# Optimization experiments

Measured on AMD Instinct MI355X. Metric: run time of the kernel, lower is better.

The kernel has to match this reference:

```python
import jax, jax.numpy as jnp
import numpy as np
from math import factorial

# ---- config (matches init_kwargs) ----
N = 50000                 # batch of nodes/edges
LS = [0, 1, 2]            # l of each irrep block (in1, in2, out all share this)
MUL1, MUL2, MULO = 128, 1, 128
DIM = sum(2 * l + 1 for l in LS)  # 9 basis functions
INSTR = [(0,0,0),(0,1,1),(0,2,2),(1,0,1),(1,1,0),(1,1,1),(1,1,2),(1,2,1),(1,2,2),
         (2,0,2),(2,1,1),(2,1,2),(2,2,0),(2,2,1),(2,2,2)]
PATH_NUMEL = MUL1 * MUL2 * MULO   # uvw path shape
WEIGHT_NUMEL = len(INSTR) * PATH_NUMEL

# ---- Wigner 3j (real basis, e3nn convention) computed once in numpy ----

def _su2_cg(j1, m1, j2, m2, j3, m3):
    if m3 != m1 + m2:
        return 0.0
    vmin = int(max(-j1 + j2 + m3, -j1 + m1, 0))
    vmax = int(min(j2 + j3 + m1, j3 - j1 + j2, j3 + m3))
    f = lambda n: factorial(int(round(n)))
    C = ((2*j3+1) * f(j3+j1-j2) * f(j3-j1+j2) * f(j1+j2-j3) / f(j1+j2+j3+1)
         * f(j3+m3) * f(j3-m3) / (f(j1-m1)*f(j1+m1)*f(j2-m2)*f(j2+m2))) ** 0.5
    S = 0.0
    for v in range(vmin, vmax + 1):
        S += (-1.0)**(v + j2 + m2) / f(v) * f(j2+j3+m1-v) * f(j1-m1+v) / (
            f(j3-j1+j2-v) * f(j3+m3-v) * f(v+j1-j2-m3))
    return C * S

def _su2_clebsch_gordan(j1, j2, j3):
    mat = np.zeros((2*j1+1, 2*j2+1, 2*j3+1))
    for i, m1 in enumerate(range(-j1, j1+1)):
        for j, m2 in enumerate(range(-j2, j2+1)):
            for k, m3 in enumerate(range(-j3, j3+1)):
                mat[i, j, k] = _su2_cg(j1, m1, j2, m2, j3, m3)
    return mat

def _change_basis_real_to_complex(l):
    q = np.zeros((2*l+1, 2*l+1), dtype=np.complex128)
    for m in range(-l, 0):
        q[l+m, l+abs(m)] = 1/np.sqrt(2)
        q[l+m, l-abs(m)] = -1j/np.sqrt(2)
    q[l, l] = 1.0
    for m in range(1, l+1):
        q[l+m, l+abs(m)] = (-1)**m/np.sqrt(2)
        q[l+m, l-abs(m)] = 1j*(-1)**m/np.sqrt(2)
    return (-1j)**l * q

def wigner_3j(l1, l2, l3):
    C = _su2_clebsch_gordan(l1, l2, l3).astype(np.complex128)
    Q1 = _change_basis_real_to_complex(l1)
    Q2 = _change_basis_real_to_complex(l2)
    Q3 = _change_basis_real_to_complex(l3)
    C = np.einsum('ij,kl,mn,ikn->jlm', Q1, Q2, np.conj(Q3.T), C)
    assert np.abs(C.imag).max() < 1e-9
    C = C.real
    return C / np.linalg.norm(C)

_W3J = {}
for (i1, i2, io) in INSTR:
    key = (LS[i1], LS[i2], LS[io])
    if key not in _W3J:
        _W3J[key] = wigner_3j(*key).astype(np.float32)

# ---- normalization coefficients (irrep_normalization='component',
#      path_normalization='element', path_weight=1, path_weight_sqrt) ----
_ALPHA = []
for (i1, i2, io) in INSTR:
    x = sum(MUL1 * MUL2 for (_, _, c) in INSTR if c == io)  # num_elements per out
    _ALPHA.append(float(np.sqrt((2 * LS[io] + 1) / x)))

# per-l slices into the basis dim
_SLICES = []
_i = 0
for l in LS:
    _SLICES.append(slice(_i, _i + 2*l + 1))
    _i += 2*l + 1


def _forward(x1, x2, weight):
    # x1: (N, 9, MUL1) channel-last; x2: (N, 9, MUL2); weight: (WEIGHT_NUMEL,)
    x1_list = [x1[:, s, :] for s in _SLICES]
    x2_list = [x2[:, s, :] for s in _SLICES]
    outs = [[] for _ in LS]
    fw = 0
    for (i1, i2, io), alpha in zip(INSTR, _ALPHA):
        w = weight[fw:fw + PATH_NUMEL].reshape(MUL1, MUL2, MULO)[:, 0, :]  # squeeze v=1
        fw += PATH_NUMEL
        w3j = jnp.asarray(_W3J[(LS[i1], LS[i2], LS[io])], dtype=x1.dtype)
        # uvw branch: xx = einsum('ziu,zjv,ijk->zku'), then matmul with (u, w_out)
        xx = jnp.einsum('ziu,zjv,ijk->zku', x1_list[i1], x2_list[i2], w3j)
        outs[io].append(alpha * jnp.matmul(xx, w))  # (N, 2*l_out+1, MULO)
    summed = [o[0] if len(o) == 1 else sum(o[1:], o[0]) for o in outs]
    return jnp.concatenate(summed, axis=1)  # (N, 9, MULO)


def setup_inputs() -> dict:
    key = jax.random.key(0)
    k1, k2, k3 = jax.random.split(key, 3)
    return {
        'x1': jax.random.normal(k1, (N, DIM, MUL1), jnp.float32),
        'x2': jax.random.normal(k2, (N, DIM, MUL2), jnp.float32),
        'weight': jax.random.normal(k3, (WEIGHT_NUMEL,), jnp.float32),
    }


def reference(x1, x2, weight):
    return _forward(x1, x2, weight)
```

## Files before the change

kernel.cpp:

```cpp
#include <hip/hip_runtime.h>
#include <cmath>
#include <complex>
#include <vector>
#include <algorithm>

#define DEVFN __device__ __forceinline__

typedef short short8 __attribute__((ext_vector_type(8)));
typedef float f32x4  __attribute__((ext_vector_type(4)));

namespace {

constexpr int NNODE  = 50000;
constexpr int TILE_Z = 16;
constexpr int NBLOCK = NNODE / TILE_Z;
static_assert(NBLOCK * TILE_Z == NNODE, "tile");

constexpr int I_L1[15] = {0,0,0,1,1,1,1,1,1,2,2,2,2,2,2};
constexpr int I_L2[15] = {0,1,2,0,1,1,1,2,2,0,1,1,2,2,2};
constexpr int I_LO[15] = {0,1,2,1,0,1,2,1,2,2,1,2,0,1,2};
constexpr int W3OFF[15] = {0,1,10,35,44,53,80,125,170,245,270,315,390,415,490};
constexpr int LOFF[3] = {0,1,4};

struct TPParams { float w3j[615]; };
struct AlphaArg { float a[15]; };

double ffact(int n){ double r=1.0; for(int i=2;i<=n;++i) r*=i; return r; }

double su2cg(int j1,int m1,int j2,int m2,int j3,int m3){
  if(m3 != m1+m2) return 0.0;
  int vmin = std::max(std::max(-j1+j2+m3, -j1+m1), 0);
  int vmax = std::min(std::min(j2+j3+m1, j3-j1+j2), j3+m3);
  double C = std::sqrt((2.0*j3+1.0)*ffact(j3+j1-j2)*ffact(j3-j1+j2)*ffact(j1+j2-j3)
             /ffact(j1+j2+j3+1)
             *ffact(j3+m3)*ffact(j3-m3)
             /(ffact(j1-m1)*ffact(j1+m1)*ffact(j2-m2)*ffact(j2+m2)));
  double S = 0.0;
  for(int v=vmin; v<=vmax; ++v){
    double t = ffact(j2+j3+m1-v)*ffact(j1-m1+v)
             /(ffact(v)*ffact(j3-j1+j2-v)*ffact(j3+m3-v)*ffact(v+j1-j2-m3));
    S += ((v+j2+m2)&1) ? -t : t;
  }
  return C*S;
}

void cbasis(int l, std::complex<double>* q){
  int n = 2*l+1;
  for(int i=0;i<n*n;++i) q[i] = std::complex<double>(0.0,0.0);
  const double is2 = 1.0/std::sqrt(2.0);
  for(int m=-l; m<0; ++m){
    q[(l+m)*n + (l-m)] = std::complex<double>(is2, 0.0);
    q[(l+m)*n + (l+m)] = std::complex<double>(0.0, -is2);
  }
  q[l*n+l] = std::complex<double>(1.0, 0.0);
  for(int m=1; m<=l; ++m){
    double s = (m&1) ? -1.0 : 1.0;
    q[(l+m)*n + (l+m)] = std::complex<double>(s*is2, 0.0);
    q[(l+m)*n + (l-m)] = std::complex<double>(0.0, s*is2);
  }
  std::complex<double> ph;
  switch(l&3){ case 0: ph = std::complex<double>(1,0);  break;
               case 1: ph = std::complex<double>(0,-1); break;
               case 2: ph = std::complex<double>(-1,0); break;
               default: ph = std::complex<double>(0,1);  break; }
  for(int i=0;i<n*n;++i) q[i] *= ph;
}

void wigner3j_tab(int l1,int l2,int l3, float* dst){
  int n1=2*l1+1, n2=2*l2+1, n3=2*l3+1;
  std::vector<double> C(n1*n2*n3);
  for(int i=0;i<n1;++i) for(int k=0;k<n2;++k) for(int n=0;n<n3;++n)
    C[(i*n2+k)*n3+n] = su2cg(l1,i-l1, l2,k-l2, l3,n-l3);
  std::vector<std::complex<double>> Q1(n1*n1), Q2(n2*n2), Q3(n3*n3);
  cbasis(l1,Q1.data()); cbasis(l2,Q2.data()); cbasis(l3,Q3.data());
  std::vector<double> R(n1*n2*n3, 0.0);
  for(int j=0;j<n1;++j) for(int l=0;l<n2;++l) for(int m=0;m<n3;++m){
    std::complex<double> s(0,0);
    for(int i=0;i<n1;++i) for(int k=0;k<n2;++k) for(int n=0;n<n3;++n)
      s += Q1[i*n1+j]*Q2[k*n2+l]*std::conj(Q3[n*n3+m])*C[(i*n2+k)*n3+n];
    R[(j*n2+l)*n3+m] = s.real();
  }
  double nrm=0; for(double v:R) nrm += v*v; nrm = std::sqrt(nrm);
  for(int t=0;t<n1*n2*n3;++t) dst[t] = (float)(R[t]/nrm);
}

void fill_params(TPParams& P, AlphaArg& A){
  for(int ins=0; ins<15; ++ins)
    wigner3j_tab(I_L1[ins], I_L2[ins], I_LO[ins], P.w3j + W3OFF[ins]);
  int cnt[3] = {0,0,0};
  for(int ins=0; ins<15; ++ins) cnt[I_LO[ins]]++;
  for(int ins=0; ins<15; ++ins){
    int lo = I_LO[ins];
    A.a[ins] = (float)std::sqrt((2.0*lo+1.0)/(128.0*cnt[lo]));
  }
}

}

DEVFN unsigned f2bf(float f){
  unsigned u = __float_as_uint(f);
  return (u + 0x7fffu + ((u>>16)&1u)) >> 16;
}
DEVFN unsigned pkbf(float a, float b){ return f2bf(a) | (f2bf(b)<<16); }

template<typename T, typename F>
DEVFN T bc(F f){ static_assert(sizeof(T)==sizeof(F), "size"); T t; __builtin_memcpy(&t,&f,sizeof(T)); return t; }

__global__ __launch_bounds__(256)
void prep_kernel(const float* __restrict__ w, unsigned short* __restrict__ ws,
                 AlphaArg al)
{
  int t = blockIdx.x*256 + threadIdx.x;
  int p = t >> 14, rem = t & 16383, u = rem >> 7, col = rem & 127;
  float v = w[t] * al.a[p];
  int gs = (u>>3) ^ (col & 15);
  ws[(p<<14) + (col<<7) + (gs<<3) + (u&7)] = (unsigned short)f2bf(v);
}

template<int INS>
DEVFN void path_phaseA(const TPParams& P, const unsigned x1p[9][4],
                       const float x2r[9], uint4* sxxU4, int z, int ug)
{
  constexpr int L1 = I_L1[INS], L2 = I_L2[INS], LO = I_LO[INS];
  constexpr int N1 = 2*L1+1, N2 = 2*L2+1, NO = 2*LO+1;
  constexpr int O1 = LOFF[L1], O2 = LOFF[L2], W3 = W3OFF[INS];

  float cc[NO][N1];
  #pragma unroll
  for(int k=0;k<NO;++k){
    #pragma unroll
    for(int i=0;i<N1;++i){
      float s = 0.f;
      #pragma unroll
      for(int j=0;j<N2;++j)
        s += P.w3j[W3 + (i*N2+j)*NO + k] * x2r[O2 + j];
      cc[k][i] = s;
    }
  }
  float a8[NO][8];
  #pragma unroll
  for(int k=0;k<NO;++k){
    #pragma unroll
    for(int e=0;e<8;++e) a8[k][e]=0.f;
  }
  #pragma unroll
  for(int i=0;i<N1;++i){
    float xf[8];
    #pragma unroll
    for(int pr=0;pr<4;++pr){
      unsigned u = x1p[O1+i][pr];
      xf[2*pr]   = __uint_as_float(u << 16);
      xf[2*pr+1] = __uint_as_float(u & 0xffff0000u);
    }
    #pragma unroll
    for(int k=0;k<NO;++k){
      #pragma unroll
      for(int e=0;e<8;++e) a8[k][e] += cc[k][i]*xf[e];
    }
  }
  #pragma unroll
  for(int k=0;k<NO;++k){
    uint4 o;
    o.x = pkbf(a8[k][0], a8[k][1]);
    o.y = pkbf(a8[k][2], a8[k][3]);
    o.z = pkbf(a8[k][4], a8[k][5]);
    o.w = pkbf(a8[k][6], a8[k][7]);
    sxxU4[(k*16 + z)*16 + ((ug ^ z) & 15)] = o;
  }
}

template<int INS>
DEVFN void path_gemm(const uint4* sxxU4, const uint4* sWTU4,
                     f32x4 (*acc)[2], int lane, int wv)
{
  constexpr int LO = I_LO[INS], NO = 2*LO+1;
  const int m = lane & 15, q = lane >> 4;
  #pragma unroll
  for(int ks=0; ks<4; ++ks){
    const int g  = ks*4 + q;
    const int gp = (g ^ m) & 15;
    short8 a[NO];
    #pragma unroll
    for(int k=0;k<NO;++k)
      a[k] = bc<short8>(sxxU4[(k*16 + m)*16 + gp]);
    #pragma unroll
    for(int ct=0; ct<2; ++ct){
      const int w = (wv*2 + ct)*16 + m;
      short8 b = bc<short8>(sWTU4[w*16 + gp]);
      #pragma unroll
      for(int k=0;k<NO;++k)
        acc[k][ct] = __builtin_amdgcn_mfma_f32_16x16x32_bf16(a[k], b, acc[k][ct], 0,0,0);
    }
  }
}

DEVFN void stage_wt(const uint4* __restrict__ wsrc, uint4* sWT, int tid){
  typedef __attribute__((address_space(1))) const void gvoid;
  typedef __attribute__((address_space(3))) void lvoid;
  #pragma unroll
  for(int r=0;r<8;++r){
    gvoid* gp = (gvoid*)(wsrc + r*256 + tid);
    lvoid* lp = (lvoid*)(sWT  + r*256 + tid);
    __builtin_amdgcn_global_load_lds(gp, lp, 16, 0, 0);
  }
}

template<int LO, int NO>
DEVFN void write_out(float* __restrict__ out, long zbase,
                     const f32x4 (*acc)[2], int lane, int wv)
{
  constexpr int OO = LOFF[LO];
  const int col = lane & 15, q = lane >> 4;
  #pragma unroll
  for(int k=0;k<NO;++k){
    #pragma unroll
    for(int ct=0;ct<2;++ct){
      #pragma unroll
      for(int r=0;r<4;++r)
        out[(zbase + q*4 + r)*1152 + (OO+k)*128 + (wv*2 + ct)*16 + col] = acc[k][ct][r];
    }
  }
}

__global__ __launch_bounds__(256, 3)
void tp_kernel(const float* __restrict__ x1, const float* __restrict__ x2,
               const unsigned short* __restrict__ wsb, float* __restrict__ out,
               TPParams P)
{
  __shared__ uint4 sxxU4[5*16*16];
  __shared__ uint4 sWTU4[2048];

  const int tid = threadIdx.x;
  const long zbase = (long)blockIdx.x * TILE_Z;
  const int z = tid >> 4, ug = tid & 15;
  const int lane = tid & 63, wv = tid >> 6;

  unsigned x1p[9][4];
  float x2r[9];
  {
    const float* xsrc = x1 + (zbase + z)*1152 + ug*8;
    #pragma unroll
    for(int i=0;i<9;++i){
      float4 a = *reinterpret_cast<const float4*>(xsrc + i*128);
      float4 b = *reinterpret_cast<const float4*>(xsrc + i*128 + 4);
      x1p[i][0] = pkbf(a.x, a.y); x1p[i][1] = pkbf(a.z, a.w);
      x1p[i][2] = pkbf(b.x, b.y); x1p[i][3] = pkbf(b.z, b.w);
    }
    #pragma unroll
    for(int j=0;j<9;++j) x2r[j] = x2[(zbase + z)*9 + j];
  }

  const uint4* wsbU4 = reinterpret_cast<const uint4*>(wsb);

#define DO_PATH(n, ACC)                                          \
  stage_wt(wsbU4 + (n)*2048, sWTU4, tid);                        \
  path_phaseA<n>(P, x1p, x2r, sxxU4, z, ug);                     \
  __syncthreads();                                               \
  path_gemm<n>(sxxU4, sWTU4, ACC, lane, wv);                     \
  __syncthreads();

  {
    f32x4 a0[1][2];
    #pragma unroll
    for(int c=0;c<2;++c){ f32x4 zz = {0.f,0.f,0.f,0.f}; a0[0][c] = zz; }
    DO_PATH(0,  a0)
    DO_PATH(4,  a0)
    DO_PATH(12, a0)
    write_out<0,1>(out, zbase, a0, lane, wv);
  }

  {
    f32x4 a1[3][2];
    #pragma unroll
    for(int k=0;k<3;++k){
      #pragma unroll
      for(int c=0;c<2;++c){ f32x4 zz = {0.f,0.f,0.f,0.f}; a1[k][c] = zz; }
    }
    DO_PATH(1,  a1)
    DO_PATH(3,  a1)
    DO_PATH(5,  a1)
    DO_PATH(7,  a1)
    DO_PATH(10, a1)
    DO_PATH(13, a1)
    write_out<1,3>(out, zbase, a1, lane, wv);
  }

  {
    f32x4 a2[5][2];
    #pragma unroll
    for(int k=0;k<5;++k){
      #pragma unroll
      for(int c=0;c<2;++c){ f32x4 zz = {0.f,0.f,0.f,0.f}; a2[k][c] = zz; }
    }
    DO_PATH(2,  a2)
    DO_PATH(6,  a2)
    DO_PATH(8,  a2)
    DO_PATH(9,  a2)
    DO_PATH(11, a2)
    DO_PATH(14, a2)
    write_out<2,5>(out, zbase, a2, lane, wv);
  }
#undef DO_PATH
}

extern "C" void kernel_launch(void* const* d_in, const int* in_sizes, int n_in,
                              void* d_out, int out_size, void* d_ws, size_t ws_size,
                              hipStream_t stream)
{
  (void)in_sizes; (void)n_in; (void)out_size; (void)ws_size;
  const float* x1 = (const float*)d_in[0];
  const float* x2 = (const float*)d_in[1];
  const float* wt = (const float*)d_in[2];
  float* out = (float*)d_out;
  unsigned short* wsb = (unsigned short*)d_ws;

  static TPParams P;
  static AlphaArg A;
  static bool inited = false;
  if(!inited){ fill_params(P, A); inited = true; }

  prep_kernel<<<dim3(960), dim3(256), 0, stream>>>(wt, wsb, A);
  tp_kernel<<<dim3(NBLOCK), dim3(256), 0, stream>>>(x1, x2, wsb, out, P);
}
```

Baseline: 507.6 us.

## Software-pipeline weight staging and phase A with double-buffered xx tiles

Restructures the per-path loop into epochs. In each epoch the current weight tile is read from LDS into registers, the next path's weight tile is prefetched into LDS via global_load_lds, and the MFMA GEMM for the current path runs while phase A for the next path writes into a second xx buffer. This replaces two __syncthreads per path with one manual barrier and uses s_setprio to favour the MFMA section. It doubles the xx LDS footprint, keeps the B fragments in registers, and lowers launch bounds from 3 to 2 blocks per CU, which may reduce occupancy.

```diff
diff --git a/kernel.cpp b/kernel.cpp
--- a/kernel.cpp
+++ b/kernel.cpp
@@ -169,38 +169,52 @@
   }
 }
 
+DEVFN void path_gemm_pre(const uint4* sWTU4, short8 bfr[2][4], int lane, int wv){
+  const int m = lane & 15, q = lane >> 4;
+  #pragma unroll
+  for(int ks=0; ks<4; ++ks){
+    const int gp = ((ks*4 + q) ^ m) & 15;
+    #pragma unroll
+    for(int ct=0; ct<2; ++ct){
+      const int w = (wv*2 + ct)*16 + m;
+      bfr[ct][ks] = bc<short8>(sWTU4[w*16 + gp]);
+    }
+  }
+}
+
 template<int INS>
-DEVFN void path_gemm(const uint4* sxxU4, const uint4* sWTU4,
-                     f32x4 (*acc)[2], int lane, int wv)
-{
-  constexpr int LO = I_LO[INS], NO = 2*LO+1;
+DEVFN void path_gemm_mfma(const uint4* sxxU4, const short8 bfr[2][4],
+                          f32x4 (*acc)[2], int lane)
+{
+  constexpr int NO = 2*I_LO[INS]+1;
   const int m = lane & 15, q = lane >> 4;
+  __builtin_amdgcn_s_setprio(1);
   #pragma unroll
   for(int ks=0; ks<4; ++ks){
-    const int g  = ks*4 + q;
-    const int gp = (g ^ m) & 15;
+    const int gp = ((ks*4 + q) ^ m) & 15;
     short8 a[NO];
     #pragma unroll
     for(int k=0;k<NO;++k)
       a[k] = bc<short8>(sxxU4[(k*16 + m)*16 + gp]);
     #pragma unroll
     for(int ct=0; ct<2; ++ct){
-      const int w = (wv*2 + ct)*16 + m;
-      short8 b = bc<short8>(sWTU4[w*16 + gp]);
       #pragma unroll
       for(int k=0;k<NO;++k)
-        acc[k][ct] = __builtin_amdgcn_mfma_f32_16x16x32_bf16(a[k], b, acc[k][ct], 0,0,0);
-    }
-  }
-}
-
-DEVFN void stage_wt(const uint4* __restrict__ wsrc, uint4* sWT, int tid){
+        acc[k][ct] = __builtin_amdgcn_mfma_f32_16x16x32_bf16(a[k], bfr[ct][ks], acc[k][ct], 0,0,0);
+    }
+  }
+  __builtin_amdgcn_s_setprio(0);
+}
+
+DEVFN void stage_wt_wave(const uint4* __restrict__ wsrc, uint4* sWT,
+                         int wv, int lane){
   typedef __attribute__((address_space(1))) const void gvoid;
   typedef __attribute__((address_space(3))) void lvoid;
   #pragma unroll
   for(int r=0;r<8;++r){
-    gvoid* gp = (gvoid*)(wsrc + r*256 + tid);
-    lvoid* lp = (lvoid*)(sWT  + r*256 + tid);
+    const int off = wv*512 + r*64 + lane;
+    gvoid* gp = (gvoid*)(wsrc + off);
+    lvoid* lp = (lvoid*)(sWT  + off);
     __builtin_amdgcn_global_load_lds(gp, lp, 16, 0, 0);
   }
 }
@@ -222,18 +236,31 @@
   }
 }
 
-__global__ __launch_bounds__(256, 3)
+template<int NK>
+DEVFN void zacc(f32x4 (*a)[2]){
+  #pragma unroll
+  for(int k=0;k<NK;++k){
+    #pragma unroll
+    for(int c=0;c<2;++c){ f32x4 zz = {0.f,0.f,0.f,0.f}; a[k][c] = zz; }
+  }
+}
+
+__global__ __launch_bounds__(256, 2)
 void tp_kernel(const float* __restrict__ x1, const float* __restrict__ x2,
                const unsigned short* __restrict__ wsb, float* __restrict__ out,
                TPParams P)
 {
-  __shared__ uint4 sxxU4[5*16*16];
+  __shared__ uint4 sxx[2][5*16*16];
   __shared__ uint4 sWTU4[2048];
 
   const int tid = threadIdx.x;
   const long zbase = (long)blockIdx.x * TILE_Z;
   const int z = tid >> 4, ug = tid & 15;
   const int lane = tid & 63, wv = tid >> 6;
+
+  const uint4* wsbU4 = reinterpret_cast<const uint4*>(wsb);
+
+  stage_wt_wave(wsbU4 + 0*2048, sWTU4, wv, lane);
 
   unsigned x1p[9][4];
   float x2r[9];
@@ -250,57 +277,62 @@
     for(int j=0;j<9;++j) x2r[j] = x2[(zbase + z)*9 + j];
   }
 
-  const uint4* wsbU4 = reinterpret_cast<const uint4*>(wsb);
-
-#define DO_PATH(n, ACC)                                          \
-  stage_wt(wsbU4 + (n)*2048, sWTU4, tid);                        \
-  path_phaseA<n>(P, x1p, x2r, sxxU4, z, ug);                     \
-  __syncthreads();                                               \
-  path_gemm<n>(sxxU4, sWTU4, ACC, lane, wv);                     \
-  __syncthreads();
-
-  {
-    f32x4 a0[1][2];
-    #pragma unroll
-    for(int c=0;c<2;++c){ f32x4 zz = {0.f,0.f,0.f,0.f}; a0[0][c] = zz; }
-    DO_PATH(0,  a0)
-    DO_PATH(4,  a0)
-    DO_PATH(12, a0)
-    write_out<0,1>(out, zbase, a0, lane, wv);
-  }
-
-  {
-    f32x4 a1[3][2];
-    #pragma unroll
-    for(int k=0;k<3;++k){
-      #pragma unroll
-      for(int c=0;c<2;++c){ f32x4 zz = {0.f,0.f,0.f,0.f}; a1[k][c] = zz; }
-    }
-    DO_PATH(1,  a1)
-    DO_PATH(3,  a1)
-    DO_PATH(5,  a1)
-    DO_PATH(7,  a1)
-    DO_PATH(10, a1)
-    DO_PATH(13, a1)
-    write_out<1,3>(out, zbase, a1, lane, wv);
-  }
-
-  {
-    f32x4 a2[5][2];
-    #pragma unroll
-    for(int k=0;k<5;++k){
-      #pragma unroll
-      for(int c=0;c<2;++c){ f32x4 zz = {0.f,0.f,0.f,0.f}; a2[k][c] = zz; }
-    }
-    DO_PATH(2,  a2)
-    DO_PATH(6,  a2)
-    DO_PATH(8,  a2)
-    DO_PATH(9,  a2)
-    DO_PATH(11, a2)
-    DO_PATH(14, a2)
-    write_out<2,5>(out, zbase, a2, lane, wv);
-  }
-#undef DO_PATH
+  path_phaseA<0>(P, x1p, x2r, sxx[0], z, ug);
+  asm volatile("s_waitcnt lgkmcnt(0)" ::: "memory");
+  __builtin_amdgcn_s_barrier();
+
+#define EPOCH(CUR, NXT, ACC, EB)                                          \
+  {                                                                       \
+    asm volatile("s_waitcnt vmcnt(0)" ::: "memory");     \
+    __builtin_amdgcn_sched_barrier(0);                                    \
+    short8 bfr[2][4];                                                     \
+    path_gemm_pre(sWTU4, bfr, lane, wv);                                  \
+    asm volatile("s_waitcnt lgkmcnt(0)" ::: "memory"); \
+    __builtin_amdgcn_sched_barrier(0);                                    \
+    stage_wt_wave(wsbU4 + (NXT)*2048, sWTU4, wv, lane);                   \
+    path_gemm_mfma<CUR>(sxx[EB], bfr, ACC, lane);                         \
+    path_phaseA<NXT>(P, x1p, x2r, sxx[(EB)^1], z, ug);                    \
+    asm volatile("s_waitcnt lgkmcnt(0)" ::: "memory"); \
+    __builtin_amdgcn_s_barrier();                                         \
+  }
+
+#define EPOCH_LAST(CUR, ACC, EB)                                          \
+  {                                                                       \
+    asm volatile("s_waitcnt vmcnt(0)" ::: "memory");                      \
+    __builtin_amdgcn_sched_barrier(0);                                    \
+    short8 bfr[2][4];                                                     \
+    path_gemm_pre(sWTU4, bfr, lane, wv);                                  \
+    path_gemm_mfma<CUR>(sxx[EB], bfr, ACC, lane);                         \
+  }
+
+  f32x4 a0[1][2], a1[3][2], a2[5][2];
+
+  zacc<1>(a0);
+  EPOCH(0,  4,  a0, 0)
+  EPOCH(4,  12, a0, 1)
+  EPOCH(12, 1,  a0, 0)
+  write_out<0,1>(out, zbase, a0, lane, wv);
+
+  zacc<3>(a1);
+  EPOCH(1,  3,  a1, 1)
+  EPOCH(3,  5,  a1, 0)
+  EPOCH(5,  7,  a1, 1)
+  EPOCH(7,  10, a1, 0)
+  EPOCH(10, 13, a1, 1)
+  EPOCH(13, 2,  a1, 0)
+  write_out<1,3>(out, zbase, a1, lane, wv);
+
+  zacc<5>(a2);
+  EPOCH(2,  6,  a2, 1)
+  EPOCH(6,  8,  a2, 0)
+  EPOCH(8,  9,  a2, 1)
+  EPOCH(9,  11, a2, 0)
+  EPOCH(11, 14, a2, 1)
+  EPOCH_LAST(14, a2, 0)
+  write_out<2,5>(out, zbase, a2, lane, wv);
+
+#undef EPOCH
+#undef EPOCH_LAST
 }
 
 extern "C" void kernel_launch(void* const* d_in, const int* in_sizes, int n_in,
```

After: 1.205 ms. +137.5%, slower.
